# Optimization experiments

Measured on AMD Instinct MI355X. Metric: run time of the kernel, lower is better.

The kernel has to match this reference:

```python
import jax, jax.numpy as jnp
import numpy as np

NUM_SEGMENTS = 4
SIZE_SEG = 2  # sqrt(num_segments)


def conv2d_same(x, w, b):
    # x: [B,C,H,W], w: [O,I,3,3], padding=1, stride=1
    y = jax.lax.conv_general_dilated(
        x, w, window_strides=(1, 1), padding=((1, 1), (1, 1)),
        dimension_numbers=("NCHW", "OIHW", "NCHW"))
    return y + b[None, :, None, None]


def setup_inputs() -> dict:
    key = jax.random.key(0)
    k1, k2, k3, k4, k5 = jax.random.split(key, 5)
    B, C, H, W = 4, 64, 512, 512
    x = jax.random.normal(k1, (B, C, H, W), dtype=jnp.float32)
    # Conv params (kaiming-ish small scale)
    local_w = jax.random.normal(k2, (NUM_SEGMENTS, NUM_SEGMENTS, 3, 3), dtype=jnp.float32) * 0.1
    local_b = jax.random.normal(k3, (NUM_SEGMENTS,), dtype=jnp.float32) * 0.01
    global_w = jax.random.normal(k4, (1, 2, 3, 3), dtype=jnp.float32) * 0.1
    global_b = jax.random.normal(k5, (1,), dtype=jnp.float32) * 0.01
    return {"x": x, "local_w": local_w, "local_b": local_b,
            "global_w": global_w, "global_b": global_b}


def local_attention(x, w, b):
    B, C, H, W = x.shape
    s = SIZE_SEG
    Hs, Ws = H // s, W // s
    # L2 norm over channel dim, keepdim -> [B,1,H,W]
    l2 = jnp.sqrt(jnp.sum(x * x, axis=1, keepdims=True))
    # Split into s*s spatial tiles, stacked on channel dim in (i,j) row-major order
    # [B,1,H,W] -> [B,s,Hs,s,Ws] -> [B,s,s,Hs,Ws] -> [B,s*s,Hs,Ws]
    tiles = l2[:, 0].reshape(B, s, Hs, s, Ws).transpose(0, 1, 3, 2, 4).reshape(B, s * s, Hs, Ws)
    out = jax.nn.sigmoid(conv2d_same(tiles, w, b))  # [B, s*s, Hs, Ws]
    # torch: chunk along ch, cat along dim2, view(l2.shape) == flat row-major reshape
    return out.reshape(B, 1, H, W)


def global_attention(x, w, b):
    max_out = jnp.max(x, axis=1, keepdims=True)
    mean_out = jnp.mean(x, axis=1, keepdims=True)
    cat = jnp.concatenate([max_out, mean_out], axis=1)  # [B,2,H,W]
    return jax.nn.sigmoid(jax.nn.relu(conv2d_same(cat, w, b)))


def reference(x, local_w, local_b, global_w, global_b):
    return local_attention(x, local_w, local_b) + global_attention(x, global_w, global_b)
```

## Files before the change

kernel.cpp:

```cpp
#include <hip/hip_runtime.h>
#include <math.h>

#define HH 512
#define WW 512
#define HW (HH * WW)
#define CCH 64
#define BB 4
#define C_RES 48

typedef float    f4 __attribute__((ext_vector_type(4)));
typedef _Float16 h2 __attribute__((ext_vector_type(2)));
typedef _Float16 h4 __attribute__((ext_vector_type(4)));
typedef _Float16 h8 __attribute__((ext_vector_type(8)));

__global__ __launch_bounds__(256) void reduce_k(const float* __restrict__ x,
                                                _Float16* __restrict__ l2p,
                                                h2* __restrict__ mmp) {
    int tid = blockIdx.x * 256 + threadIdx.x;
    int b  = tid >> 16;
    int p4 = tid & 65535;

    const f4* xb = reinterpret_cast<const f4*>(x)
                 + (size_t)b * CCH * (HW / 4) + p4;

    f4 ss = {0.f, 0.f, 0.f, 0.f};
    f4 sm = {0.f, 0.f, 0.f, 0.f};
    f4 mx = {-INFINITY, -INFINITY, -INFINITY, -INFINITY};

#pragma unroll 8
    for (int c = 0; c < C_RES; ++c) {
        f4 v = xb[(size_t)c * (HW / 4)];
        ss += v * v;
        sm += v;
        mx.x = fmaxf(mx.x, v.x);
        mx.y = fmaxf(mx.y, v.y);
        mx.z = fmaxf(mx.z, v.z);
        mx.w = fmaxf(mx.w, v.w);
    }
#pragma unroll 8
    for (int c = C_RES; c < CCH; ++c) {
        f4 v = __builtin_nontemporal_load(xb + (size_t)c * (HW / 4));
        ss += v * v;
        sm += v;
        mx.x = fmaxf(mx.x, v.x);
        mx.y = fmaxf(mx.y, v.y);
        mx.z = fmaxf(mx.z, v.z);
        mx.w = fmaxf(mx.w, v.w);
    }

    size_t o4 = (size_t)b * (HW / 4) + p4;
    const float inv = 1.0f / 64.0f;

    h8 mm = { (_Float16)mx.x, (_Float16)(sm.x * inv),
              (_Float16)mx.y, (_Float16)(sm.y * inv),
              (_Float16)mx.z, (_Float16)(sm.z * inv),
              (_Float16)mx.w, (_Float16)(sm.w * inv) };
    h4 l2v = { (_Float16)sqrtf(ss.x), (_Float16)sqrtf(ss.y),
               (_Float16)sqrtf(ss.z), (_Float16)sqrtf(ss.w) };
    reinterpret_cast<h8*>(mmp)[o4] = mm;
    reinterpret_cast<h4*>(l2p)[o4] = l2v;
}

__global__ __launch_bounds__(256) void attn_k(const _Float16* __restrict__ l2p,
                                              const h2* __restrict__ mmp,
                                              const float* __restrict__ lw,
                                              const float* __restrict__ lb,
                                              const float* __restrict__ gw,
                                              const float* __restrict__ gb,
                                              float* __restrict__ out) {
    __shared__ float s_lw[144];
    __shared__ float s_lb[4];
    __shared__ float s_gw[18];
    __shared__ float s_gb;

    int t = threadIdx.x;
    if (t < 144) s_lw[t] = lw[t];
    if (t < 4)   s_lb[t] = lb[t];
    if (t < 18)  s_gw[t] = gw[t];
    if (t == 0)  s_gb = gb[0];
    __syncthreads();

    int idx4 = blockIdx.x * 256 + t;
    int b  = idx4 >> 16;
    int p4 = idx4 & 65535;
    int h  = p4 >> 7;
    int w0 = (p4 & 127) << 2;

    const _Float16* l2b = l2p + ((size_t)b << 18);
    const h2*       mmb = mmp + ((size_t)b << 18);

    float g0 = s_gb, g1 = s_gb, g2 = s_gb, g3 = s_gb;
#pragma unroll
    for (int dh = -1; dh <= 1; ++dh) {
        int hh = h + dh;
        if ((unsigned)hh >= (unsigned)HH) continue;
        const h2* row = mmb + hh * WW + w0;
        h8 v = *reinterpret_cast<const h8*>(row);
        float m6[6], a6[6];
        if (w0 > 0) { h2 e = row[-1]; m6[0] = (float)e.x; a6[0] = (float)e.y; }
        else        { m6[0] = 0.f;    a6[0] = 0.f; }
        m6[1] = (float)v[0]; a6[1] = (float)v[1];
        m6[2] = (float)v[2]; a6[2] = (float)v[3];
        m6[3] = (float)v[4]; a6[3] = (float)v[5];
        m6[4] = (float)v[6]; a6[4] = (float)v[7];
        if (w0 < WW - 4) { h2 e = row[4]; m6[5] = (float)e.x; a6[5] = (float)e.y; }
        else             { m6[5] = 0.f;   a6[5] = 0.f; }
#pragma unroll
        for (int k = 0; k < 3; ++k) {
            float wmk = s_gw[(dh + 1) * 3 + k];
            float wak = s_gw[9 + (dh + 1) * 3 + k];
            g0 = fmaf(m6[0 + k], wmk, fmaf(a6[0 + k], wak, g0));
            g1 = fmaf(m6[1 + k], wmk, fmaf(a6[1 + k], wak, g1));
            g2 = fmaf(m6[2 + k], wmk, fmaf(a6[2 + k], wak, g2));
            g3 = fmaf(m6[3 + k], wmk, fmaf(a6[3 + k], wak, g3));
        }
    }

    int c   = h >> 7;
    int hs  = ((h & 127) << 1) | (w0 >> 8);
    int ws0 = w0 & 255;

    float la0 = s_lb[c], la1 = la0, la2 = la0, la3 = la0;
#pragma unroll
    for (int i = 0; i < 4; ++i) {
        const _Float16* base = l2b + (i >> 1) * (256 * WW) + (i & 1) * 256;
        const float* wi = s_lw + c * 36 + i * 9;
#pragma unroll
        for (int dh = -1; dh <= 1; ++dh) {
            int y = hs + dh;
            if ((unsigned)y >= 256u) continue;
            const _Float16* row = base + y * WW + ws0;
            h4 v = *reinterpret_cast<const h4*>(row);
            float v6[6];
            v6[0] = (ws0 > 0)   ? (float)row[-1] : 0.f;
            v6[1] = (float)v[0]; v6[2] = (float)v[1];
            v6[3] = (float)v[2]; v6[4] = (float)v[3];
            v6[5] = (ws0 < 252) ? (float)row[4]  : 0.f;
#pragma unroll
            for (int k = 0; k < 3; ++k) {
                float wk = wi[(dh + 1) * 3 + k];
                la0 = fmaf(v6[0 + k], wk, la0);
                la1 = fmaf(v6[1 + k], wk, la1);
                la2 = fmaf(v6[2 + k], wk, la2);
                la3 = fmaf(v6[3 + k], wk, la3);
            }
        }
    }

    f4 o;
    o.x = 1.f / (1.f + __expf(-la0)) + 1.f / (1.f + __expf(-fmaxf(g0, 0.f)));
    o.y = 1.f / (1.f + __expf(-la1)) + 1.f / (1.f + __expf(-fmaxf(g1, 0.f)));
    o.z = 1.f / (1.f + __expf(-la2)) + 1.f / (1.f + __expf(-fmaxf(g2, 0.f)));
    o.w = 1.f / (1.f + __expf(-la3)) + 1.f / (1.f + __expf(-fmaxf(g3, 0.f)));
    __builtin_nontemporal_store(o, reinterpret_cast<f4*>(out) + idx4);
}

extern "C" void kernel_launch(void* const* d_in, const int* in_sizes, int n_in,
                              void* d_out, int out_size, void* d_ws, size_t ws_size,
                              hipStream_t stream) {
    const float* x  = (const float*)d_in[0];
    const float* lw = (const float*)d_in[1];
    const float* lb = (const float*)d_in[2];
    const float* gw = (const float*)d_in[3];
    const float* gb = (const float*)d_in[4];
    float* out = (float*)d_out;

    h2*       mmp = (h2*)d_ws;
    _Float16* l2p = (_Float16*)((char*)d_ws + (size_t)BB * HW * sizeof(h2));

    int n1 = BB * HW / 4;
    reduce_k<<<n1 / 256, 256, 0, stream>>>(x, l2p, mmp);

    int n2 = BB * HW / 4;
    attn_k<<<n2 / 256, 256, 0, stream>>>(l2p, mmp, lw, lb, gw, gb, out);
}
```

Measured before the change: 58.77 us.

## Fuse reduction and attention kernels with a software grid barrier

Merges the channel-reduction kernel and the attention/conv kernel into one launch of 1024 blocks. The two phases are separated by an atomic-counter grid barrier with sleep-spinning, and a memset resets the counter. The goal is to remove the second kernel's launch gap and tail, and the reduction loop also drops its nontemporal loads. The risks: correctness depends on all blocks being co-resident (hence the launch bounds), the spin has a timeout that could silently break the barrier, and the memset adds its own launch.

```diff
diff --git a/kernel.cpp b/kernel.cpp
--- a/kernel.cpp
+++ b/kernel.cpp
@@ -6,68 +6,22 @@
 #define HW (HH * WW)
 #define CCH 64
 #define BB 4
-#define C_RES 48
+#define NBLOCKS (BB * HW / 4 / 256)
 
 typedef float    f4 __attribute__((ext_vector_type(4)));
 typedef _Float16 h2 __attribute__((ext_vector_type(2)));
 typedef _Float16 h4 __attribute__((ext_vector_type(4)));
 typedef _Float16 h8 __attribute__((ext_vector_type(8)));
 
-__global__ __launch_bounds__(256) void reduce_k(const float* __restrict__ x,
-                                                _Float16* __restrict__ l2p,
-                                                h2* __restrict__ mmp) {
-    int tid = blockIdx.x * 256 + threadIdx.x;
-    int b  = tid >> 16;
-    int p4 = tid & 65535;
-
-    const f4* xb = reinterpret_cast<const f4*>(x)
-                 + (size_t)b * CCH * (HW / 4) + p4;
-
-    f4 ss = {0.f, 0.f, 0.f, 0.f};
-    f4 sm = {0.f, 0.f, 0.f, 0.f};
-    f4 mx = {-INFINITY, -INFINITY, -INFINITY, -INFINITY};
-
-#pragma unroll 8
-    for (int c = 0; c < C_RES; ++c) {
-        f4 v = xb[(size_t)c * (HW / 4)];
-        ss += v * v;
-        sm += v;
-        mx.x = fmaxf(mx.x, v.x);
-        mx.y = fmaxf(mx.y, v.y);
-        mx.z = fmaxf(mx.z, v.z);
-        mx.w = fmaxf(mx.w, v.w);
-    }
-#pragma unroll 8
-    for (int c = C_RES; c < CCH; ++c) {
-        f4 v = __builtin_nontemporal_load(xb + (size_t)c * (HW / 4));
-        ss += v * v;
-        sm += v;
-        mx.x = fmaxf(mx.x, v.x);
-        mx.y = fmaxf(mx.y, v.y);
-        mx.z = fmaxf(mx.z, v.z);
-        mx.w = fmaxf(mx.w, v.w);
-    }
-
-    size_t o4 = (size_t)b * (HW / 4) + p4;
-    const float inv = 1.0f / 64.0f;
-
-    h8 mm = { (_Float16)mx.x, (_Float16)(sm.x * inv),
-              (_Float16)mx.y, (_Float16)(sm.y * inv),
-              (_Float16)mx.z, (_Float16)(sm.z * inv),
-              (_Float16)mx.w, (_Float16)(sm.w * inv) };
-    h4 l2v = { (_Float16)sqrtf(ss.x), (_Float16)sqrtf(ss.y),
-               (_Float16)sqrtf(ss.z), (_Float16)sqrtf(ss.w) };
-    reinterpret_cast<h8*>(mmp)[o4] = mm;
-    reinterpret_cast<h4*>(l2p)[o4] = l2v;
-}
-
-__global__ __launch_bounds__(256) void attn_k(const _Float16* __restrict__ l2p,
-                                              const h2* __restrict__ mmp,
-                                              const float* __restrict__ lw,
-                                              const float* __restrict__ lb,
-                                              const float* __restrict__ gw,
-                                              const float* __restrict__ gb,
-                                              float* __restrict__ out) {
+__global__ __launch_bounds__(256, 4) void fused_k(const float* __restrict__ x,
+                                                  _Float16* __restrict__ l2p,
+                                                  h2* __restrict__ mmp,
+                                                  unsigned* __restrict__ barrier_cnt,
+                                                  const float* __restrict__ lw,
+                                                  const float* __restrict__ lb,
+                                                  const float* __restrict__ gw,
+                                                  const float* __restrict__ gb,
+                                                  float* __restrict__ out) {
     __shared__ float s_lw[144];
     __shared__ float s_lb[4];
     __shared__ float s_gw[18];
@@ -78,13 +32,57 @@
     if (t < 4)   s_lb[t] = lb[t];
     if (t < 18)  s_gw[t] = gw[t];
     if (t == 0)  s_gb = gb[0];
+
+    int tid = blockIdx.x * 256 + t;
+    int b   = tid >> 16;
+    int p4i = tid & 65535;
+
+    {
+        const f4* xb = reinterpret_cast<const f4*>(x)
+                     + (size_t)b * CCH * (HW / 4) + p4i;
+
+        f4 ss = {0.f, 0.f, 0.f, 0.f};
+        f4 sm = {0.f, 0.f, 0.f, 0.f};
+        f4 mx = {-INFINITY, -INFINITY, -INFINITY, -INFINITY};
+
+#pragma unroll 8
+        for (int c = 0; c < CCH; ++c) {
+            f4 v = xb[(size_t)c * (HW / 4)];
+            ss += v * v;
+            sm += v;
+            mx.x = fmaxf(mx.x, v.x);
+            mx.y = fmaxf(mx.y, v.y);
+            mx.z = fmaxf(mx.z, v.z);
+            mx.w = fmaxf(mx.w, v.w);
+        }
+
+        size_t o4 = (size_t)b * (HW / 4) + p4i;
+        const float inv = 1.0f / 64.0f;
+        h8 mm = { (_Float16)mx.x, (_Float16)(sm.x * inv),
+                  (_Float16)mx.y, (_Float16)(sm.y * inv),
+                  (_Float16)mx.z, (_Float16)(sm.z * inv),
+                  (_Float16)mx.w, (_Float16)(sm.w * inv) };
+        h4 l2v = { (_Float16)sqrtf(ss.x), (_Float16)sqrtf(ss.y),
+                   (_Float16)sqrtf(ss.z), (_Float16)sqrtf(ss.w) };
+        reinterpret_cast<h8*>(mmp)[o4] = mm;
+        reinterpret_cast<h4*>(l2p)[o4] = l2v;
+    }
+
+    __syncthreads();
+    if (t == 0) {
+        __hip_atomic_fetch_add(barrier_cnt, 1u, __ATOMIC_ACQ_REL,
+                               __HIP_MEMORY_SCOPE_AGENT);
+        int spins = 0;
+        while (__hip_atomic_load(barrier_cnt, __ATOMIC_ACQUIRE,
+                                 __HIP_MEMORY_SCOPE_AGENT) < (unsigned)NBLOCKS) {
+            __builtin_amdgcn_s_sleep(64);
+            if (++spins > (1 << 18)) break;
+        }
+    }
     __syncthreads();
 
-    int idx4 = blockIdx.x * 256 + t;
-    int b  = idx4 >> 16;
-    int p4 = idx4 & 65535;
-    int h  = p4 >> 7;
-    int w0 = (p4 & 127) << 2;
+    int h  = p4i >> 7;
+    int w0 = (p4i & 127) << 2;
 
     const _Float16* l2b = l2p + ((size_t)b << 18);
     const h2*       mmb = mmp + ((size_t)b << 18);
@@ -152,7 +150,7 @@
     o.y = 1.f / (1.f + __expf(-la1)) + 1.f / (1.f + __expf(-fmaxf(g1, 0.f)));
     o.z = 1.f / (1.f + __expf(-la2)) + 1.f / (1.f + __expf(-fmaxf(g2, 0.f)));
     o.w = 1.f / (1.f + __expf(-la3)) + 1.f / (1.f + __expf(-fmaxf(g3, 0.f)));
-    __builtin_nontemporal_store(o, reinterpret_cast<f4*>(out) + idx4);
+    __builtin_nontemporal_store(o, reinterpret_cast<f4*>(out) + tid);
 }
 
 extern "C" void kernel_launch(void* const* d_in, const int* in_sizes, int n_in,
@@ -167,10 +165,10 @@
 
     h2*       mmp = (h2*)d_ws;
     _Float16* l2p = (_Float16*)((char*)d_ws + (size_t)BB * HW * sizeof(h2));
+    unsigned* cnt = (unsigned*)((char*)d_ws + (size_t)BB * HW * 6);
 
-    int n1 = BB * HW / 4;
-    reduce_k<<<n1 / 256, 256, 0, stream>>>(x, l2p, mmp);
+    hipMemsetAsync(cnt, 0, sizeof(unsigned), stream);
 
-    int n2 = BB * HW / 4;
-    attn_k<<<n2 / 256, 256, 0, stream>>>(l2p, mmp, lw, lb, gw, gb, out);
+    fused_k<<<NBLOCKS, 256, 0, stream>>>(x, l2p, mmp, cnt,
+                                         lw, lb, gw, gb, out);
 }
```

Result: slower. 184.5 us (+214.0%).
